# Performance work log

Measured on AMD Instinct MI355X. Metric: run time of the kernel, lower is better.

The kernel has to match this reference:

```python
import jax, jax.numpy as jnp
import numpy as np
import math

NUM_HEADS = 8

def setup_inputs() -> dict:
    key = jax.random.key(0)
    ks = jax.random.split(key, 20)
    N, n, M, E = 4096, 3, 16, 256
    nE = 65536
    s = lambda k, shape: (jax.random.normal(k, shape, jnp.float32) * 0.02)
    return {
        "equ": jax.random.normal(ks[0], (N, n, M), jnp.float32),
        "h": jax.random.normal(ks[1], (N, E), jnp.float32),
        "edge_index": jax.random.randint(ks[2], (2, nE), 0, N),
        "edge_fea": jax.random.normal(ks[3], (nE, 4), jnp.float32),
        "W_equ": s(ks[4], (M, E)),
        "W_gproj": s(ks[5], (E, 32)),
        "W_vg": s(ks[6], (E, E)),
        "W_g1": s(ks[7], (32 * 32, 2 * E)), "b_g1": jnp.zeros((2 * E,), jnp.float32),
        "W_g2": s(ks[8], (2 * E, E)), "b_g2": jnp.zeros((E,), jnp.float32),
        "W_q": s(ks[9], (2 * E, E)), "b_q": jnp.zeros((E,), jnp.float32),
        "W_k": s(ks[10], (2 * E, E)), "b_k": jnp.zeros((E,), jnp.float32),
        "W_v": s(ks[11], (2 * E, E)), "b_v": jnp.zeros((E,), jnp.float32),
        "W_ng": s(ks[12], (E, E)), "b_ng": jnp.zeros((E,), jnp.float32),
        "W_gout": s(ks[13], (E, E)),
        "W_gdec": s(ks[14], (E, M)),
        "W_hdec": s(ks[15], (E, E)), "b_hdec": jnp.zeros((E,), jnp.float32),
    }


def reference(equ, h, edge_index, edge_fea, W_equ, W_gproj, W_vg, W_g1, b_g1,
              W_g2, b_g2, W_q, b_q, W_k, b_k, W_v, b_v, W_ng, b_ng,
              W_gout, W_gdec, W_hdec, b_hdec):
    # edge_index / edge_fea are unused in the original forward (dead args).
    N, n, M = equ.shape
    E = W_equ.shape[1]
    H = NUM_HEADS
    D = E // H
    scaling = D ** -0.5
    sqrtE = math.sqrt(E)

    g_src = (equ @ W_equ) * sqrtE                     # [N, n, E]
    h_src = h * sqrtE                                 # [N, E]

    g2 = g_src @ W_gproj                              # [N, n, 32]
    gram = jnp.einsum('nia,nib->nab', g2, g2)         # [N, 32, 32]
    g2 = gram.reshape(N, 32 * 32)
    g2 = jax.nn.relu(g2 @ W_g1 + b_g1) @ W_g2 + b_g2  # [N, E]

    h2 = jnp.concatenate([g2, h_src], axis=-1)        # [N, 2E]
    q = ((h2 @ W_q + b_q) * scaling).reshape(N, H, D)
    k = (h2 @ W_k + b_k).reshape(N, H, D)
    v = (h2 @ W_v + b_v).reshape(N, H, D)
    vg = (g_src @ W_vg).reshape(N, n, H, D)           # [N, n, H, D]

    attn = jax.nn.softmax(jnp.einsum('nhd,mhd->hnm', q, k), axis=-1)  # [H, N, N]

    out_v = jnp.einsum('hnm,mhd->nhd', attn, v).reshape(N, E)
    h_src1 = out_v @ W_ng + b_ng                      # [N, E]

    # Same attention probs reused for the vector channel (torch does repeat+bmm;
    # we broadcast instead of materializing the repeated [n*H, N, N] tensor).
    out_g = jnp.einsum('hnm,mvhd->nvhd', attn, vg).reshape(N, n, E)
    g_src1 = out_g @ W_gout                           # [N, n, E]

    g_src = g_src + g_src1
    h_src = h_src + h_src1
    equ_out = g_src @ W_gdec                          # [N, n, M]
    h_out = h_src @ W_hdec + b_hdec                   # [N, E]
    return (equ_out, h_out)
```

## Files before the change

### kernel.cpp

```cpp
#include <hip/hip_runtime.h>
#include <hip/hip_bf16.h>

typedef __attribute__((ext_vector_type(8))) short short8;
typedef __attribute__((ext_vector_type(4))) float floatx4;

constexpr int N_ = 4096;
constexpr float SQRT_E = 16.0f;
constexpr float QSCALE = 0.17677669529663687f * 1.4426950408889634f;

__device__ __forceinline__ ushort f2bf(float x) {
  __hip_bfloat16 h = __float2bfloat16(x);
  return *reinterpret_cast<ushort*>(&h);
}
__device__ __forceinline__ float bf2f(ushort b) {
  unsigned int u = ((unsigned int)b) << 16;
  return __uint_as_float(u);
}

__device__ __forceinline__ float dpp_max16(float x) {
  int v = __float_as_int(x);
  int y;
  y = __builtin_amdgcn_update_dpp(v, v, 0x128, 0xf, 0xf, false);
  v = __float_as_int(fmaxf(__int_as_float(v), __int_as_float(y)));
  y = __builtin_amdgcn_update_dpp(v, v, 0x124, 0xf, 0xf, false);
  v = __float_as_int(fmaxf(__int_as_float(v), __int_as_float(y)));
  y = __builtin_amdgcn_update_dpp(v, v, 0x122, 0xf, 0xf, false);
  v = __float_as_int(fmaxf(__int_as_float(v), __int_as_float(y)));
  y = __builtin_amdgcn_update_dpp(v, v, 0x121, 0xf, 0xf, false);
  v = __float_as_int(fmaxf(__int_as_float(v), __int_as_float(y)));
  return __int_as_float(v);
}

__device__ __forceinline__ void do_transpose(
    const float* __restrict__ src, ushort* __restrict__ dsth,
    ushort* __restrict__ dstl, int R, int C, int lb, int cb_shift,
    float* smem, int hasLo)
{
  float (*tile)[33] = (float(*)[33])smem;
  const int r0 = (lb >> cb_shift) * 32;
  const int c0 = (lb & ((1 << cb_shift) - 1)) * 32;
  const int tx = threadIdx.x & 31, ty = threadIdx.x >> 5;
  #pragma unroll
  for (int p = 0; p < 4; ++p) {
    const int lr = p*8 + ty;
    tile[lr][tx] = (r0+lr < R && c0+tx < C) ? src[(size_t)(r0+lr)*C + c0 + tx] : 0.f;
  }
  __syncthreads();
  #pragma unroll
  for (int p = 0; p < 4; ++p) {
    const int dc = p*8 + ty;
    if (c0+dc < C && r0+tx < R) {
      const float v = tile[tx][dc];
      const ushort hi = f2bf(v);
      dsth[(size_t)(c0+dc)*R + r0 + tx] = hi;
      if (hasLo) dstl[(size_t)(c0+dc)*R + r0 + tx] = f2bf(v - bf2f(hi));
    }
  }
}

__global__ __launch_bounds__(256) void k_prep(
    const float* __restrict__ equ, const float* __restrict__ h,
    const float* __restrict__ W_equ, const float* __restrict__ W_gproj,
    const float* __restrict__ W_g1, const float* __restrict__ W_g2,
    const float* __restrict__ W_q, const float* __restrict__ W_k,
    const float* __restrict__ W_v, const float* __restrict__ W_vg,
    const float* __restrict__ W_ng, const float* __restrict__ W_gout,
    const float* __restrict__ W_hdec, const float* __restrict__ W_gdec,
    ushort* __restrict__ Wg1t, ushort* __restrict__ Wg2t,
    ushort* __restrict__ Wth, ushort* __restrict__ Wtl,
    ushort* __restrict__ Wvgt, ushort* __restrict__ Wngt,
    ushort* __restrict__ Wgoutt, ushort* __restrict__ Whdect,
    ushort* __restrict__ Wgdect,
    ushort* __restrict__ h2h, ushort* __restrict__ h2l,
    ushort* __restrict__ vt,
    ushort* __restrict__ g_src_b, ushort* __restrict__ gram_b)
{
  __shared__ __align__(16) float smem[1056];
  const int b = blockIdx.x;
  const int t = threadIdx.x;

  if (b < 512) {
    do_transpose(W_g1, Wg1t, nullptr, 1024, 512, b, 4, smem, 0);
  } else if (b < 640) {
    do_transpose(W_g2, Wg2t, nullptr, 512, 256, b-512, 3, smem, 0);
  } else if (b < 768) {
    do_transpose(W_q, Wth, Wtl, 512, 256, b-640, 3, smem, 1);
  } else if (b < 896) {
    do_transpose(W_k, Wth + 256*512, Wtl + 256*512, 512, 256, b-768, 3, smem, 1);
  } else if (b < 1024) {
    do_transpose(W_v, Wth + 512*512, Wtl + 512*512, 512, 256, b-896, 3, smem, 1);
  } else if (b < 1088) {
    do_transpose(W_vg, Wvgt, nullptr, 256, 256, b-1024, 3, smem, 0);
  } else if (b < 1152) {
    do_transpose(W_ng, Wngt, nullptr, 256, 256, b-1088, 3, smem, 0);
  } else if (b < 1216) {
    do_transpose(W_gout, Wgoutt, nullptr, 256, 256, b-1152, 3, smem, 0);
  } else if (b < 1280) {
    do_transpose(W_hdec, Whdect, nullptr, 256, 256, b-1216, 3, smem, 0);
  } else if (b < 1288) {
    do_transpose(W_gdec, Wgdect, nullptr, 256, 16, b-1280, 0, smem, 0);
  } else if (b < 5384) {
    const int i = b - 1288;
    const float v = h[(size_t)i*256 + t] * SQRT_E;
    const ushort hi = f2bf(v);
    h2h[(size_t)i*512 + 256 + t] = hi;
    h2l[(size_t)i*512 + 256 + t] = f2bf(v - bf2f(hi));
  } else if (b < 7432) {
    const int idx = (b - 5384)*256 + t;
    const int n = idx & 4095;
    const int c16 = (idx >> 12) & 15;
    const int hh = idx >> 16;
    vt[((size_t)hh*144 + 128 + c16)*N_ + n] = (c16 == 0) ? (ushort)0x3F80 : (ushort)0;
  } else {
    float* eq  = smem;
    float* gs  = smem + 48;
    float* g2p = smem + 816;
    const int i = b - 7432;
    if (t < 48) eq[t] = equ[(size_t)i*48 + t];
    __syncthreads();
    #pragma unroll
    for (int j = 0; j < 3; ++j) {
      float s = 0.f;
      #pragma unroll
      for (int m = 0; m < 16; ++m) s += eq[j*16+m] * W_equ[m*256 + t];
      s *= SQRT_E;
      gs[j*256 + t] = s;
      g_src_b[((size_t)i*3 + j)*256 + t] = f2bf(s);
    }
    __syncthreads();
    if (t < 96) {
      const int j = t >> 5, a = t & 31;
      float s = 0.f;
      for (int e = 0; e < 256; ++e) s += gs[j*256+e] * W_gproj[e*32 + a];
      g2p[t] = s;
    }
    __syncthreads();
    #pragma unroll
    for (int r = 0; r < 4; ++r) {
      const int idx = r*256 + t;
      const int a = idx >> 5, bb = idx & 31;
      const float s = g2p[a]*g2p[bb] + g2p[32+a]*g2p[32+bb] + g2p[64+a]*g2p[64+bb];
      gram_b[(size_t)i*1024 + idx] = f2bf(s);
    }
  }
}

template<int KTOT>
__device__ __forceinline__ void gemm_core(
    const ushort* __restrict__ A, const ushort* __restrict__ Bt,
    int bM, int bN, floatx4 acc[4], ushort* As, ushort* Bs)
{
  const int t = threadIdx.x;
  const int wave = t >> 6, lane = t & 63, quad = lane >> 4, m = lane & 15;
  #pragma unroll
  for (int ct = 0; ct < 4; ++ct) acc[ct] = {0.f, 0.f, 0.f, 0.f};
  const int row = t >> 2, kq = (t & 3) * 8;
  for (int k0 = 0; k0 < KTOT; k0 += 32) {
    __syncthreads();
    *(short8*)&As[row*40 + kq] = *(const short8*)&A[(size_t)(bM+row)*KTOT + k0 + kq];
    *(short8*)&Bs[row*40 + kq] = *(const short8*)&Bt[(size_t)(bN+row)*KTOT + k0 + kq];
    __syncthreads();
    const short8 af = *(const short8*)&As[(wave*16 + m)*40 + quad*8];
    #pragma unroll
    for (int ct = 0; ct < 4; ++ct) {
      const short8 bf = *(const short8*)&Bs[(ct*16 + m)*40 + quad*8];
      acc[ct] = __builtin_amdgcn_mfma_f32_16x16x32_bf16(af, bf, acc[ct], 0, 0, 0);
    }
  }
}

template<int KTOT>
__device__ __forceinline__ void gemm_core3(
    const ushort* __restrict__ Ah, const ushort* __restrict__ Al,
    const ushort* __restrict__ Bth, const ushort* __restrict__ Btl,
    int bM, int bN, floatx4 acc[4],
    ushort* Ash, ushort* Asl, ushort* Bsh, ushort* Bsl)
{
  const int t = threadIdx.x;
  const int wave = t >> 6, lane = t & 63, quad = lane >> 4, m = lane & 15;
  #pragma unroll
  for (int ct = 0; ct < 4; ++ct) acc[ct] = {0.f, 0.f, 0.f, 0.f};
  const int row = t >> 2, kq = (t & 3) * 8;
  for (int k0 = 0; k0 < KTOT; k0 += 32) {
    __syncthreads();
    *(short8*)&Ash[row*40 + kq] = *(const short8*)&Ah[(size_t)(bM+row)*KTOT + k0 + kq];
    *(short8*)&Asl[row*40 + kq] = *(const short8*)&Al[(size_t)(bM+row)*KTOT + k0 + kq];
    *(short8*)&Bsh[row*40 + kq] = *(const short8*)&Bth[(size_t)(bN+row)*KTOT + k0 + kq];
    *(short8*)&Bsl[row*40 + kq] = *(const short8*)&Btl[(size_t)(bN+row)*KTOT + k0 + kq];
    __syncthreads();
    const short8 ah = *(const short8*)&Ash[(wave*16 + m)*40 + quad*8];
    const short8 al = *(const short8*)&Asl[(wave*16 + m)*40 + quad*8];
    #pragma unroll
    for (int ct = 0; ct < 4; ++ct) {
      const short8 bh = *(const short8*)&Bsh[(ct*16 + m)*40 + quad*8];
      const short8 bl = *(const short8*)&Bsl[(ct*16 + m)*40 + quad*8];
      acc[ct] = __builtin_amdgcn_mfma_f32_16x16x32_bf16(ah, bl, acc[ct], 0, 0, 0);
      acc[ct] = __builtin_amdgcn_mfma_f32_16x16x32_bf16(al, bh, acc[ct], 0, 0, 0);
      acc[ct] = __builtin_amdgcn_mfma_f32_16x16x32_bf16(ah, bh, acc[ct], 0, 0, 0);
    }
  }
}

__global__ __launch_bounds__(256) void k_g1(
    const ushort* __restrict__ gram_b, const ushort* __restrict__ Wg1t,
    const float* __restrict__ b_g1, ushort* __restrict__ hidden)
{
  __shared__ __align__(16) ushort As[64*40], Bs[64*40];
  floatx4 acc[4];
  const int bM = blockIdx.x*64, bN = blockIdx.y*64;
  gemm_core<1024>(gram_b, Wg1t, bM, bN, acc, As, Bs);
  const int lane = threadIdx.x & 63, wave = threadIdx.x >> 6;
  const int quad = lane >> 4, m = lane & 15;
  #pragma unroll
  for (int ct = 0; ct < 4; ++ct) {
    const int c = bN + ct*16 + m;
    #pragma unroll
    for (int r = 0; r < 4; ++r) {
      const int i = bM + wave*16 + quad*4 + r;
      hidden[(size_t)i*512 + c] = f2bf(fmaxf(acc[ct][r] + b_g1[c], 0.f));
    }
  }
}

__global__ __launch_bounds__(256) void k_g2(
    const ushort* __restrict__ hidden, const ushort* __restrict__ Wg2t,
    const float* __restrict__ b_g2, ushort* __restrict__ h2h, ushort* __restrict__ h2l)
{
  __shared__ __align__(16) ushort As[64*40], Bs[64*40];
  floatx4 acc[4];
  const int bM = blockIdx.x*64, bN = blockIdx.y*64;
  gemm_core<512>(hidden, Wg2t, bM, bN, acc, As, Bs);
  const int lane = threadIdx.x & 63, wave = threadIdx.x >> 6;
  const int quad = lane >> 4, m = lane & 15;
  #pragma unroll
  for (int ct = 0; ct < 4; ++ct) {
    const int c = bN + ct*16 + m;
    #pragma unroll
    for (int r = 0; r < 4; ++r) {
      const int i = bM + wave*16 + quad*4 + r;
      const float s = acc[ct][r] + b_g2[c];
      const ushort hi = f2bf(s);
      h2h[(size_t)i*512 + c] = hi;
      h2l[(size_t)i*512 + c] = f2bf(s - bf2f(hi));
    }
  }
}

__global__ __launch_bounds__(256) void k_g34(
    const ushort* __restrict__ h2h, const ushort* __restrict__ h2l,
    const ushort* __restrict__ Wth, const ushort* __restrict__ Wtl,
    const float* __restrict__ b_q, const float* __restrict__ b_k,
    const float* __restrict__ b_v,
    const ushort* __restrict__ g_src_b, const ushort* __restrict__ Wvgt,
    float* __restrict__ q_ws, ushort* __restrict__ kh, ushort* __restrict__ kl,
    ushort* __restrict__ vt)
{
  __shared__ __align__(16) ushort S0[64*40], S1[64*40], S2[64*40], S3[64*40];
  const int lb = blockIdx.y*192 + blockIdx.x;
  const int lane = threadIdx.x & 63, wave = threadIdx.x >> 6;
  const int quad = lane >> 4, m = lane & 15;
  floatx4 acc[4];
  if (lb < 768) {
    const int bM = (lb & 63)*64, bN = (lb >> 6)*64;
    gemm_core3<512>(h2h, h2l, Wth, Wtl, bM, bN, acc, S0, S1, S2, S3);
    #pragma unroll
    for (int ct = 0; ct < 4; ++ct) {
      const int c = bN + ct*16 + m;
      #pragma unroll
      for (int r = 0; r < 4; ++r) {
        const int i = bM + wave*16 + quad*4 + r;
        if (c < 256) {
          const float s = acc[ct][r] + b_q[c];
          q_ws[((size_t)(c >> 5)*N_ + i)*32 + (c & 31)] = s * QSCALE;
        } else if (c < 512) {
          const int cc = c - 256;
          const float s = acc[ct][r] + b_k[cc];
          const ushort hi = f2bf(s);
          kh[((size_t)(cc >> 5)*N_ + i)*32 + (cc & 31)] = hi;
          kl[((size_t)(cc >> 5)*N_ + i)*32 + (cc & 31)] = f2bf(s - bf2f(hi));
        } else {
          const int cc = c - 512;
          const float s = acc[ct][r] + b_v[cc];
          vt[((size_t)(cc >> 5)*144 + (cc & 31))*N_ + i] = f2bf(s);
        }
      }
    }
  } else {
    const int lb2 = lb - 768;
    const int bM = (lb2 >> 2)*64, bN = (lb2 & 3)*64;
    gemm_core<256>(g_src_b, Wvgt, bM, bN, acc, S0, S1);
    #pragma unroll
    for (int ct = 0; ct < 4; ++ct) {
      const int c = bN + ct*16 + m;
      const int hh = c >> 5, d = c & 31;
      #pragma unroll
      for (int r = 0; r < 4; ++r) {
        const int i3 = bM + wave*16 + quad*4 + r;
        const int i = i3 / 3, j = i3 - 3*i;
        vt[((size_t)hh*144 + 32 + j*32 + d)*N_ + i] = f2bf(acc[ct][r]);
      }
    }
  }
}

__global__ __launch_bounds__(256, 4) void k3_attn(
    const float* __restrict__ q_ws, const ushort* __restrict__ kh,
    const ushort* __restrict__ kl, const ushort* __restrict__ vt,
    ushort* __restrict__ Po0, ushort* __restrict__ Po1,
    float* __restrict__ Pml)
{
  __shared__ __align__(16) ushort Khs[64*40], Kls[64*40];
  __shared__ __align__(16) ushort Vs[144*64];
  __shared__ __align__(16) ushort Pl[4*16*72];
  __shared__ float li_s[64];

  const int t    = threadIdx.x;
  const int wave = t >> 6;
  const int lane = t & 63;
  const int quad = lane >> 4;
  const int m    = lane & 15;
  const int h    = blockIdx.y;
  const int s    = blockIdx.z;
  const int n0q  = blockIdx.x * 64;

  union { short8 v; ushort u[8]; } Aqh, Aql;
  {
    const float* qp = q_ws + ((size_t)h*N_ + n0q + wave*16 + m)*32 + quad*8;
    #pragma unroll
    for (int jj = 0; jj < 8; ++jj) {
      const float x = qp[jj];
      const ushort hi = f2bf(x);
      Aqh.u[jj] = hi;
      Aql.u[jj] = f2bf(x - bf2f(hi));
    }
  }

  floatx4 Of[9];
  #pragma unroll
  for (int nt = 0; nt < 9; ++nt) Of[nt] = {0.f, 0.f, 0.f, 0.f};
  float mi[4];
  #pragma unroll
  for (int r = 0; r < 4; ++r) mi[r] = -3.0e38f;

  const int krow = t >> 2, kch = (t & 3) * 8;
  const int kt0 = s * 32;

  const ushort* pKh = kh + ((size_t)h*N_ + kt0*64 + krow)*32 + kch;
  const ushort* pKl = kl + ((size_t)h*N_ + kt0*64 + krow)*32 + kch;
  const ushort* pV[4];
  int wV[4];
  #pragma unroll
  for (int p = 0; p < 4; ++p) {
    const int idx = p*256 + t, row = idx >> 3, g = idx & 7;
    pV[p] = vt + ((size_t)h*144 + row)*N_ + kt0*64 + g*8;
    wV[p] = (row*8 + (g ^ (row & 7)))*8;
  }
  const ushort* pV4 = nullptr;
  int wV4 = 0;
  if (t < 128) {
    const int idx = 1024 + t, row = idx >> 3, g = idx & 7;
    pV4 = vt + ((size_t)h*144 + row)*N_ + kt0*64 + g*8;
    wV4 = (row*8 + (g ^ (row & 7)))*8;
  }

  short8 rK0 = *(const short8*)pKh;
  short8 rK1 = *(const short8*)pKl;
  short8 rV[4], rV4e;
  #pragma unroll
  for (int p = 0; p < 4; ++p) rV[p] = *(const short8*)pV[p];
  if (t < 128) rV4e = *(const short8*)pV4;

  for (int i = 0; i < 32; ++i) {
    __syncthreads();
    *(short8*)&Khs[krow*40 + kch] = rK0;
    *(short8*)&Kls[krow*40 + kch] = rK1;
    #pragma unroll
    for (int p = 0; p < 4; ++p) *(short8*)&Vs[wV[p]] = rV[p];
    if (t < 128) *(short8*)&Vs[wV4] = rV4e;
    if (i + 1 < 32) {
      pKh += 2048; pKl += 2048;
      rK0 = *(const short8*)pKh;
      rK1 = *(const short8*)pKl;
      #pragma unroll
      for (int p = 0; p < 4; ++p) { pV[p] += 64; rV[p] = *(const short8*)pV[p]; }
      if (t < 128) { pV4 += 64; rV4e = *(const short8*)pV4; }
    }
    __syncthreads();

    floatx4 sf[4];
    #pragma unroll
    for (int kb = 0; kb < 4; ++kb) {
      const short8 bkh = *(const short8*)&Khs[(kb*16 + m)*40 + quad*8];
      const short8 bkl = *(const short8*)&Kls[(kb*16 + m)*40 + quad*8];
      floatx4 sv = {0.f, 0.f, 0.f, 0.f};
      sv = __builtin_amdgcn_mfma_f32_16x16x32_bf16(Aqh.v, bkl, sv, 0, 0, 0);
      sv = __builtin_amdgcn_mfma_f32_16x16x32_bf16(Aql.v, bkh, sv, 0, 0, 0);
      sv = __builtin_amdgcn_mfma_f32_16x16x32_bf16(Aqh.v, bkh, sv, 0, 0, 0);
      sf[kb] = sv;
    }

    float tm[4];
    bool need = false;
    #pragma unroll
    for (int r = 0; r < 4; ++r) {
      float nm = fmaxf(fmaxf(sf[0][r], sf[1][r]), fmaxf(sf[2][r], sf[3][r]));
      tm[r] = dpp_max16(nm);
      need |= (tm[r] > mi[r] + 20.f);
    }
    if (__any(need)) {
      #pragma unroll
      for (int r = 0; r < 4; ++r) {
        const float mn = fmaxf(mi[r], tm[r]);
        const float al = exp2f(mi[r] - mn);
        mi[r] = mn;
        #pragma unroll
        for (int nt = 0; nt < 9; ++nt) Of[nt][r] *= al;
      }
    }
    #pragma unroll
    for (int kb = 0; kb < 4; ++kb)
      #pragma unroll
      for (int r = 0; r < 4; ++r) {
        const float pv = exp2f(sf[kb][r] - mi[r]);
        Pl[wave*1152 + (quad*4 + r)*72 + kb*16 + m] =
            (ushort)(__float_as_uint(pv) >> 16);
      }

    #pragma unroll
    for (int ks = 0; ks < 2; ++ks) {
      const short8 ap = *(const short8*)&Pl[wave*1152 + m*72 + ks*32 + quad*8];
      #pragma unroll
      for (int nt = 0; nt < 9; ++nt) {
        const int row = nt*16 + m;
        const int pos = (ks*4 + quad) ^ (row & 7);
        const short8 bv = *(const short8*)&Vs[(row*8 + pos)*8];
        Of[nt] = __builtin_amdgcn_mfma_f32_16x16x32_bf16(ap, bv, Of[nt], 0, 0, 0);
      }
    }
  }

  if (m == 0) {
    #pragma unroll
    for (int r = 0; r < 4; ++r) li_s[wave*16 + quad*4 + r] = Of[8][r];
  }
  __syncthreads();
  const floatx4 liv = *(const floatx4*)&li_s[wave*16 + quad*4];
  float linv[4];
  #pragma unroll
  for (int r = 0; r < 4; ++r) linv[r] = 1.0f / liv[r];

  ushort* Po = s ? Po1 : Po0;
  #pragma unroll
  for (int nt = 0; nt < 8; ++nt) {
    #pragma unroll
    for (int r = 0; r < 4; ++r) {
      const int n = n0q + wave*16 + quad*4 + r;
      Po[((size_t)h*N_ + n)*128 + nt*16 + m] = f2bf(Of[nt][r] * linv[r]);
    }
  }
  if (m == 0) {
    #pragma unroll
    for (int r = 0; r < 4; ++r) {
      const int n = n0q + wave*16 + quad*4 + r;
      Pml[(((size_t)s*8 + h)*N_ + n)*2 + 0] = mi[r];
      Pml[(((size_t)s*8 + h)*N_ + n)*2 + 1] = Of[8][r];
    }
  }
}

__global__ __launch_bounds__(256) void k_merge(
    const ushort* __restrict__ Po0, const ushort* __restrict__ Po1,
    const float* __restrict__ Pml,
    ushort* __restrict__ out_v_b, ushort* __restrict__ out_g_b)
{
  const int idx = blockIdx.x*256 + threadIdx.x;
  const int c0 = (idx & 15) * 8;
  const int n  = (idx >> 4) & 4095;
  const int h  = idx >> 16;
  const float m1 = Pml[(((size_t)0*8 + h)*N_ + n)*2 + 0];
  const float l1 = Pml[(((size_t)0*8 + h)*N_ + n)*2 + 1];
  const float m2 = Pml[(((size_t)1*8 + h)*N_ + n)*2 + 0];
  const float l2 = Pml[(((size_t)1*8 + h)*N_ + n)*2 + 1];
  const float M = fmaxf(m1, m2);
  const float w1 = exp2f(m1 - M) * l1;
  const float w2 = exp2f(m2 - M) * l2;
  const float inv = 1.0f / (w1 + w2);
  union { short8 v; ushort u[8]; } a, b, res;
  a.v = *(const short8*)&Po0[((size_t)h*N_ + n)*128 + c0];
  b.v = *(const short8*)&Po1[((size_t)h*N_ + n)*128 + c0];
  #pragma unroll
  for (int j = 0; j < 8; ++j)
    res.u[j] = f2bf((w1*bf2f(a.u[j]) + w2*bf2f(b.u[j])) * inv);
  if (c0 < 32) {
    *(short8*)&out_v_b[(size_t)n*256 + h*32 + c0] = res.v;
  } else {
    const int j = (c0 - 32) >> 5, cc = (c0 - 32) & 31;
    *(short8*)&out_g_b[((size_t)n*3 + j)*256 + h*32 + cc] = res.v;
  }
}

__global__ __launch_bounds__(256) void k56ab(
    const ushort* __restrict__ out_v_b, const ushort* __restrict__ Wngt,
    const float* __restrict__ b_ng, const float* __restrict__ h,
    ushort* __restrict__ tmp_b,
    const ushort* __restrict__ out_g_b, const ushort* __restrict__ Wgoutt,
    const ushort* __restrict__ g_src_b, ushort* __restrict__ gsum_b)
{
  __shared__ __align__(16) ushort As[64*40], Bs[64*40];
  floatx4 acc[4];
  const int lane = threadIdx.x & 63, wave = threadIdx.x >> 6;
  const int quad = lane >> 4, m = lane & 15;
  const int bN = blockIdx.y*64;
  if (blockIdx.x < 64) {
    const int bM = blockIdx.x*64;
    gemm_core<256>(out_v_b, Wngt, bM, bN, acc, As, Bs);
    #pragma unroll
    for (int ct = 0; ct < 4; ++ct) {
      const int c = bN + ct*16 + m;
      #pragma unroll
      for (int r = 0; r < 4; ++r) {
        const int i = bM + wave*16 + quad*4 + r;
        tmp_b[(size_t)i*256 + c] =
            f2bf(acc[ct][r] + b_ng[c] + h[(size_t)i*256 + c] * SQRT_E);
      }
    }
  } else {
    const int bM = (blockIdx.x - 64)*64;
    gemm_core<256>(out_g_b, Wgoutt, bM, bN, acc, As, Bs);
    #pragma unroll
    for (int ct = 0; ct < 4; ++ct) {
      const int c = bN + ct*16 + m;
      #pragma unroll
      for (int r = 0; r < 4; ++r) {
        const int i = bM + wave*16 + quad*4 + r;
        gsum_b[(size_t)i*256 + c] =
            f2bf(acc[ct][r] + bf2f(g_src_b[(size_t)i*256 + c]));
      }
    }
  }
}

__global__ __launch_bounds__(256) void k56cd(
    const ushort* __restrict__ tmp_b, const ushort* __restrict__ Whdect,
    const float* __restrict__ b_hdec,
    const ushort* __restrict__ gsum_b, const ushort* __restrict__ Wgdect,
    float* __restrict__ out)
{
  __shared__ __align__(16) ushort As[64*40], Bs[64*40];
  const int t = threadIdx.x;
  const int lane = t & 63, wave = t >> 6;
  const int quad = lane >> 4, m = lane & 15;
  if (blockIdx.x < 64) {
    floatx4 acc[4];
    const int bM = blockIdx.x*64, bN = blockIdx.y*64;
    gemm_core<256>(tmp_b, Whdect, bM, bN, acc, As, Bs);
    #pragma unroll
    for (int ct = 0; ct < 4; ++ct) {
      const int c = bN + ct*16 + m;
      #pragma unroll
      for (int r = 0; r < 4; ++r) {
        const int i = bM + wave*16 + quad*4 + r;
        out[196608 + (size_t)i*256 + c] = acc[ct][r] + b_hdec[c];
      }
    }
  } else if (blockIdx.y == 0) {
    const int bM = (blockIdx.x - 64)*64;
    floatx4 acc = {0.f, 0.f, 0.f, 0.f};
    const int row = t >> 2, kq = (t & 3) * 8;
    for (int k0 = 0; k0 < 256; k0 += 32) {
      __syncthreads();
      *(short8*)&As[row*40 + kq] = *(const short8*)&gsum_b[(size_t)(bM+row)*256 + k0 + kq];
      if (t < 64)
        *(short8*)&Bs[(t>>2)*40 + kq] = *(const short8*)&Wgdect[(size_t)(t>>2)*256 + k0 + kq];
      __syncthreads();
      const short8 af = *(const short8*)&As[(wave*16 + m)*40 + quad*8];
      const short8 bf = *(const short8*)&Bs[m*40 + quad*8];
      acc = __builtin_amdgcn_mfma_f32_16x16x32_bf16(af, bf, acc, 0, 0, 0);
    }
    #pragma unroll
    for (int r = 0; r < 4; ++r)
      out[(size_t)(bM + wave*16 + quad*4 + r)*16 + m] = acc[r];
  }
}

extern "C" void kernel_launch(void* const* d_in, const int* in_sizes, int n_in,
                              void* d_out, int out_size, void* d_ws, size_t ws_size,
                              hipStream_t stream) {
  const float* equ    = (const float*)d_in[0];
  const float* h      = (const float*)d_in[1];
  const float* W_equ  = (const float*)d_in[4];
  const float* W_gproj= (const float*)d_in[5];
  const float* W_vg   = (const float*)d_in[6];
  const float* W_g1   = (const float*)d_in[7];
  const float* b_g1   = (const float*)d_in[8];
  const float* W_g2   = (const float*)d_in[9];
  const float* b_g2   = (const float*)d_in[10];
  const float* W_q    = (const float*)d_in[11];
  const float* b_q    = (const float*)d_in[12];
  const float* W_k    = (const float*)d_in[13];
  const float* b_k    = (const float*)d_in[14];
  const float* W_v    = (const float*)d_in[15];
  const float* b_v    = (const float*)d_in[16];
  const float* W_ng   = (const float*)d_in[17];
  const float* b_ng   = (const float*)d_in[18];
  const float* W_gout = (const float*)d_in[19];
  const float* W_gdec = (const float*)d_in[20];
  const float* W_hdec = (const float*)d_in[21];
  const float* b_hdec = (const float*)d_in[22];
  float* out = (float*)d_out;

  char* wsb = (char*)d_ws;
  constexpr size_t MiB = 1048576;
  float*  q_ws    = (float*) (wsb +  0*MiB);
  ushort* kh      = (ushort*)(wsb +  4*MiB);
  ushort* kl      = (ushort*)(wsb +  6*MiB);
  ushort* vt      = (ushort*)(wsb +  8*MiB);
  ushort* h2h     = (ushort*)(wsb + 17*MiB);
  ushort* h2l     = (ushort*)(wsb + 21*MiB);
  ushort* g_src_b = (ushort*)(wsb + 25*MiB);
  ushort* wbase   = (ushort*)(wsb + 31*MiB);
  ushort* Wg1t = wbase;
  ushort* Wg2t = wbase + 524288;
  ushort* Wth  = wbase + 655360;
  ushort* Wtl  = wbase + 1048576;
  ushort* Wvgt = wbase + 1441792;
  ushort* wbase2  = (ushort*)(wsb + 34*MiB);
  ushort* Wngt   = wbase2;
  ushort* Wgoutt = wbase2 + 65536;
  ushort* Whdect = wbase2 + 131072;
  ushort* Wgdect = wbase2 + 196608;
  ushort* gram_b  = (ushort*)(wsb + 34*MiB + 524288);
  ushort* hidden  = (ushort*)(wsb + 42*MiB + 524288);
  ushort* Po0     = (ushort*)(wsb + 17*MiB);
  ushort* Po1     = (ushort*)(wsb + 34*MiB + 524288);
  float*  Pml     = (float*) (wsb + 47*MiB);
  ushort* out_v_b = (ushort*)(wsb +  4*MiB);
  ushort* out_g_b = (ushort*)(wsb +  8*MiB);
  ushort* tmp_b   = (ushort*)(wsb + 42*MiB + 524288);
  ushort* gsum_b  = (ushort*)(wsb + 34*MiB + 524288);

  k_prep<<<11528, 256, 0, stream>>>(
      equ, h, W_equ, W_gproj, W_g1, W_g2, W_q, W_k, W_v,
      W_vg, W_ng, W_gout, W_hdec, W_gdec,
      Wg1t, Wg2t, Wth, Wtl, Wvgt, Wngt, Wgoutt, Whdect, Wgdect,
      h2h, h2l, vt, g_src_b, gram_b);

  k_g1<<<dim3(64, 8), 256, 0, stream>>>(gram_b, Wg1t, b_g1, hidden);
  k_g2<<<dim3(64, 4), 256, 0, stream>>>(hidden, Wg2t, b_g2, h2h, h2l);
  k_g34<<<dim3(192, 8), 256, 0, stream>>>(h2h, h2l, Wth, Wtl, b_q, b_k, b_v,
                                          g_src_b, Wvgt, q_ws, kh, kl, vt);

  dim3 g3(64, 8, 2);
  k3_attn<<<g3, 256, 0, stream>>>(q_ws, kh, kl, vt, Po0, Po1, Pml);
  k_merge<<<2048, 256, 0, stream>>>(Po0, Po1, Pml, out_v_b, out_g_b);

  k56ab<<<dim3(256, 4), 256, 0, stream>>>(out_v_b, Wngt, b_ng, h, tmp_b,
                                          out_g_b, Wgoutt, g_src_b, gsum_b);
  k56cd<<<dim3(256, 4), 256, 0, stream>>>(tmp_b, Whdect, b_hdec,
                                          gsum_b, Wgdect, out);
}
```

Before: 316.9 us.

## Split attention key range three ways and use single-bf16 GEMM for V projection

The attention kernel now splits the key dimension into three chunks instead of two, launching 1536 blocks instead of 1024 to fill the GPU better. The merge kernel gains a third partial output and combines three softmax partials. Separately, the V columns of the QKV GEMM now use a single bf16 GEMM instead of the hi/lo three-product GEMM, since V is stored as bf16 anyway. This adds an extra partial-output buffer and more merge traffic, and slightly lowers V precision.

```diff
diff --git a/kernel.cpp b/kernel.cpp
--- a/kernel.cpp
+++ b/kernel.cpp
@@ -262,24 +262,34 @@
   floatx4 acc[4];
   if (lb < 768) {
     const int bM = (lb & 63)*64, bN = (lb >> 6)*64;
-    gemm_core3<512>(h2h, h2l, Wth, Wtl, bM, bN, acc, S0, S1, S2, S3);
-    #pragma unroll
-    for (int ct = 0; ct < 4; ++ct) {
-      const int c = bN + ct*16 + m;
-      #pragma unroll
-      for (int r = 0; r < 4; ++r) {
-        const int i = bM + wave*16 + quad*4 + r;
-        if (c < 256) {
-          const float s = acc[ct][r] + b_q[c];
-          q_ws[((size_t)(c >> 5)*N_ + i)*32 + (c & 31)] = s * QSCALE;
-        } else if (c < 512) {
-          const int cc = c - 256;
-          const float s = acc[ct][r] + b_k[cc];
-          const ushort hi = f2bf(s);
-          kh[((size_t)(cc >> 5)*N_ + i)*32 + (cc & 31)] = hi;
-          kl[((size_t)(cc >> 5)*N_ + i)*32 + (cc & 31)] = f2bf(s - bf2f(hi));
-        } else {
-          const int cc = c - 512;
+    if (bN < 512) {
+      gemm_core3<512>(h2h, h2l, Wth, Wtl, bM, bN, acc, S0, S1, S2, S3);
+      #pragma unroll
+      for (int ct = 0; ct < 4; ++ct) {
+        const int c = bN + ct*16 + m;
+        #pragma unroll
+        for (int r = 0; r < 4; ++r) {
+          const int i = bM + wave*16 + quad*4 + r;
+          if (c < 256) {
+            const float s = acc[ct][r] + b_q[c];
+            q_ws[((size_t)(c >> 5)*N_ + i)*32 + (c & 31)] = s * QSCALE;
+          } else {
+            const int cc = c - 256;
+            const float s = acc[ct][r] + b_k[cc];
+            const ushort hi = f2bf(s);
+            kh[((size_t)(cc >> 5)*N_ + i)*32 + (cc & 31)] = hi;
+            kl[((size_t)(cc >> 5)*N_ + i)*32 + (cc & 31)] = f2bf(s - bf2f(hi));
+          }
+        }
+      }
+    } else {
+      gemm_core<512>(h2h, Wth, bM, bN, acc, S0, S1);
+      #pragma unroll
+      for (int ct = 0; ct < 4; ++ct) {
+        const int cc = bN + ct*16 + m - 512;
+        #pragma unroll
+        for (int r = 0; r < 4; ++r) {
+          const int i = bM + wave*16 + quad*4 + r;
           const float s = acc[ct][r] + b_v[cc];
           vt[((size_t)(cc >> 5)*144 + (cc & 31))*N_ + i] = f2bf(s);
         }
@@ -306,7 +316,7 @@
 __global__ __launch_bounds__(256, 4) void k3_attn(
     const float* __restrict__ q_ws, const ushort* __restrict__ kh,
     const ushort* __restrict__ kl, const ushort* __restrict__ vt,
-    ushort* __restrict__ Po0, ushort* __restrict__ Po1,
+    ushort* __restrict__ Po0, ushort* __restrict__ Po1, ushort* __restrict__ Po2,
     float* __restrict__ Pml)
 {
   __shared__ __align__(16) ushort Khs[64*40], Kls[64*40];
@@ -323,6 +333,9 @@
   const int s    = blockIdx.z;
   const int n0q  = blockIdx.x * 64;
 
+  const int ktb = (s == 0) ? 0  : (s == 1 ? 22 : 43);
+  const int kte = (s == 0) ? 22 : (s == 1 ? 43 : 64);
+
   union { short8 v; ushort u[8]; } Aqh, Aql;
   {
     const float* qp = q_ws + ((size_t)h*N_ + n0q + wave*16 + m)*32 + quad*8;
@@ -343,23 +356,22 @@
   for (int r = 0; r < 4; ++r) mi[r] = -3.0e38f;
 
   const int krow = t >> 2, kch = (t & 3) * 8;
-  const int kt0 = s * 32;
-
-  const ushort* pKh = kh + ((size_t)h*N_ + kt0*64 + krow)*32 + kch;
-  const ushort* pKl = kl + ((size_t)h*N_ + kt0*64 + krow)*32 + kch;
+
+  const ushort* pKh = kh + ((size_t)h*N_ + ktb*64 + krow)*32 + kch;
+  const ushort* pKl = kl + ((size_t)h*N_ + ktb*64 + krow)*32 + kch;
   const ushort* pV[4];
   int wV[4];
   #pragma unroll
   for (int p = 0; p < 4; ++p) {
     const int idx = p*256 + t, row = idx >> 3, g = idx & 7;
-    pV[p] = vt + ((size_t)h*144 + row)*N_ + kt0*64 + g*8;
+    pV[p] = vt + ((size_t)h*144 + row)*N_ + ktb*64 + g*8;
     wV[p] = (row*8 + (g ^ (row & 7)))*8;
   }
   const ushort* pV4 = nullptr;
   int wV4 = 0;
   if (t < 128) {
     const int idx = 1024 + t, row = idx >> 3, g = idx & 7;
-    pV4 = vt + ((size_t)h*144 + row)*N_ + kt0*64 + g*8;
+    pV4 = vt + ((size_t)h*144 + row)*N_ + ktb*64 + g*8;
     wV4 = (row*8 + (g ^ (row & 7)))*8;
   }
 
@@ -370,14 +382,14 @@
   for (int p = 0; p < 4; ++p) rV[p] = *(const short8*)pV[p];
   if (t < 128) rV4e = *(const short8*)pV4;
 
-  for (int i = 0; i < 32; ++i) {
+  for (int kt = ktb; kt < kte; ++kt) {
     __syncthreads();
     *(short8*)&Khs[krow*40 + kch] = rK0;
     *(short8*)&Kls[krow*40 + kch] = rK1;
     #pragma unroll
     for (int p = 0; p < 4; ++p) *(short8*)&Vs[wV[p]] = rV[p];
     if (t < 128) *(short8*)&Vs[wV4] = rV4e;
-    if (i + 1 < 32) {
+    if (kt + 1 < kte) {
       pKh += 2048; pKl += 2048;
       rK0 = *(const short8*)pKh;
       rK1 = *(const short8*)pKl;
@@ -449,7 +461,7 @@
   #pragma unroll
   for (int r = 0; r < 4; ++r) linv[r] = 1.0f / liv[r];
 
-  ushort* Po = s ? Po1 : Po0;
+  ushort* Po = (s == 0) ? Po0 : ((s == 1) ? Po1 : Po2);
   #pragma unroll
   for (int nt = 0; nt < 8; ++nt) {
     #pragma unroll
@@ -470,7 +482,7 @@
 
 __global__ __launch_bounds__(256) void k_merge(
     const ushort* __restrict__ Po0, const ushort* __restrict__ Po1,
-    const float* __restrict__ Pml,
+    const ushort* __restrict__ Po2, const float* __restrict__ Pml,
     ushort* __restrict__ out_v_b, ushort* __restrict__ out_g_b)
 {
   const int idx = blockIdx.x*256 + threadIdx.x;
@@ -481,16 +493,20 @@
   const float l1 = Pml[(((size_t)0*8 + h)*N_ + n)*2 + 1];
   const float m2 = Pml[(((size_t)1*8 + h)*N_ + n)*2 + 0];
   const float l2 = Pml[(((size_t)1*8 + h)*N_ + n)*2 + 1];
-  const float M = fmaxf(m1, m2);
+  const float m3 = Pml[(((size_t)2*8 + h)*N_ + n)*2 + 0];
+  const float l3 = Pml[(((size_t)2*8 + h)*N_ + n)*2 + 1];
+  const float M = fmaxf(fmaxf(m1, m2), m3);
   const float w1 = exp2f(m1 - M) * l1;
   const float w2 = exp2f(m2 - M) * l2;
-  const float inv = 1.0f / (w1 + w2);
-  union { short8 v; ushort u[8]; } a, b, res;
+  const float w3 = exp2f(m3 - M) * l3;
+  const float inv = 1.0f / (w1 + w2 + w3);
+  union { short8 v; ushort u[8]; } a, b, c, res;
   a.v = *(const short8*)&Po0[((size_t)h*N_ + n)*128 + c0];
   b.v = *(const short8*)&Po1[((size_t)h*N_ + n)*128 + c0];
+  c.v = *(const short8*)&Po2[((size_t)h*N_ + n)*128 + c0];
   #pragma unroll
   for (int j = 0; j < 8; ++j)
-    res.u[j] = f2bf((w1*bf2f(a.u[j]) + w2*bf2f(b.u[j])) * inv);
+    res.u[j] = f2bf((w1*bf2f(a.u[j]) + w2*bf2f(b.u[j]) + w3*bf2f(c.u[j])) * inv);
   if (c0 < 32) {
     *(short8*)&out_v_b[(size_t)n*256 + h*32 + c0] = res.v;
   } else {
@@ -633,7 +649,8 @@
   ushort* hidden  = (ushort*)(wsb + 42*MiB + 524288);
   ushort* Po0     = (ushort*)(wsb + 17*MiB);
   ushort* Po1     = (ushort*)(wsb + 34*MiB + 524288);
-  float*  Pml     = (float*) (wsb + 47*MiB);
+  ushort* Po2     = (ushort*)(wsb + 42*MiB + 524288);
+  float*  Pml     = (float*) (wsb + 50*MiB + 524288);
   ushort* out_v_b = (ushort*)(wsb +  4*MiB);
   ushort* out_g_b = (ushort*)(wsb +  8*MiB);
   ushort* tmp_b   = (ushort*)(wsb + 42*MiB + 524288);
@@ -650,9 +667,9 @@
   k_g34<<<dim3(192, 8), 256, 0, stream>>>(h2h, h2l, Wth, Wtl, b_q, b_k, b_v,
                                           g_src_b, Wvgt, q_ws, kh, kl, vt);
 
-  dim3 g3(64, 8, 2);
-  k3_attn<<<g3, 256, 0, stream>>>(q_ws, kh, kl, vt, Po0, Po1, Pml);
-  k_merge<<<2048, 256, 0, stream>>>(Po0, Po1, Pml, out_v_b, out_g_b);
+  dim3 g3(64, 8, 3);
+  k3_attn<<<g3, 256, 0, stream>>>(q_ws, kh, kl, vt, Po0, Po1, Po2, Pml);
+  k_merge<<<2048, 256, 0, stream>>>(Po0, Po1, Po2, Pml, out_v_b, out_g_b);
 
   k56ab<<<dim3(256, 4), 256, 0, stream>>>(out_v_b, Wngt, b_ng, h, tmp_b,
                                           out_g_b, Wgoutt, g_src_b, gsum_b);
```

New measurement: 311.4 us. About the same (-1.7%).
